# Optimization experiments

Measured on AMD Instinct MI355X. Metric: run time of the kernel, lower is better.

## Reference

```python
import jax, jax.numpy as jnp
import numpy as np
import math

E = 1024
H = 16
D = E // H  # head_dim = 64
B, T = 2, 2048


def setup_inputs() -> dict:
    key = jax.random.key(0)
    ks = jax.random.split(key, 10)
    s_in = 1.0 / math.sqrt(E)
    s_hd = 1.0 / math.sqrt(D)
    return {
        "hidden_states": jax.random.normal(ks[0], (B, T, E), dtype=jnp.float32),
        # stacked per-head Linear weights (torch Linear: y = x @ W.T + b)
        "Wq": jax.random.uniform(ks[1], (H, E, D), jnp.float32, -s_in, s_in),
        "bq": jax.random.uniform(ks[2], (H, D), jnp.float32, -s_in, s_in),
        "Wk": jax.random.uniform(ks[3], (H, E, D), jnp.float32, -s_in, s_in),
        "bk": jax.random.uniform(ks[4], (H, D), jnp.float32, -s_in, s_in),
        "Wv": jax.random.uniform(ks[5], (H, E, D), jnp.float32, -s_in, s_in),
        "bv": jax.random.uniform(ks[6], (H, D), jnp.float32, -s_in, s_in),
        "Wo": jax.random.uniform(ks[7], (H, D, E), jnp.float32, -s_hd, s_hd),
        "bo": jax.random.uniform(ks[8], (H, E), jnp.float32, -s_hd, s_hd),
        "gate": jnp.ones((H,), dtype=jnp.float32),
    }


def reference(hidden_states, Wq, bq, Wk, bk, Wv, bv, Wo, bo, gate):
    # Batched per-head projections: [B,T,E] x [H,E,D] -> [B,H,T,D]
    Q = jnp.einsum("bte,hed->bhtd", hidden_states, Wq) + bq[None, :, None, :]
    K = jnp.einsum("bte,hed->bhtd", hidden_states, Wk) + bk[None, :, None, :]
    V = jnp.einsum("bte,hed->bhtd", hidden_states, Wv) + bv[None, :, None, :]
    scale = 1.0 / math.sqrt(D)
    scores = jnp.einsum("bhtd,bhsd->bhts", Q, K) * scale  # [B,H,T,T]
    weights = jax.nn.softmax(scores, axis=-1)
    attn = jnp.einsum("bhts,bhsd->bhtd", weights, V)  # [B,H,T,D]
    # Per-head output proj (bias included before gating), gated, summed over heads
    proj = jnp.einsum("bhtd,hde->bhte", attn, Wo) + bo[None, :, None, :]
    out = jnp.sum(proj * gate[None, :, None, None], axis=1)  # [B,T,E]
    return out
```

## Files before the change

### kernel.cpp

```cpp
#include <hip/hip_runtime.h>
#include <math.h>

#define E_DIM 1024
#define H_DIM 16
#define D_DIM 64
#define B_DIM 2
#define T_DIM 2048
#define M_TOT (B_DIM * T_DIM)

typedef __bf16 bf16_t;
typedef bf16_t bf16x4 __attribute__((ext_vector_type(4)));
typedef bf16_t bf16x8 __attribute__((ext_vector_type(8)));
typedef float f32x4 __attribute__((ext_vector_type(4)));

#define LOG2E_DIV8 0.18033688011112042f

__device__ __forceinline__ float fast_exp2(float x) {
#if __has_builtin(__builtin_amdgcn_exp2f)
    return __builtin_amdgcn_exp2f(x);
#else
    return __expf(x * 0.6931471805599453f);
#endif
}

__device__ __forceinline__ void load_lds16(const void* g, void* l) {
    __builtin_amdgcn_global_load_lds(
        (const __attribute__((address_space(1))) unsigned int*)g,
        (__attribute__((address_space(3))) unsigned int*)l, 16, 0, 0);
}

__global__ __launch_bounds__(256) void prep_kernel(
    const float* __restrict__ x,
    const float* __restrict__ Wq, const float* __restrict__ Wk,
    const float* __restrict__ Wv, const float* __restrict__ Wo,
    const float* __restrict__ bo, const float* __restrict__ gate,
    bf16_t* __restrict__ Xb, bf16_t* __restrict__ Wcat,
    bf16_t* __restrict__ Wgt, float* __restrict__ bsum) {
    __shared__ float Tt[64][65];
    const int b = blockIdx.x;
    const int tid = threadIdx.x;

    if (b < 2048) {
        size_t i = ((size_t)b * 256 + tid) * 8;
        float4 a0 = *reinterpret_cast<const float4*>(x + i);
        float4 a1 = *reinterpret_cast<const float4*>(x + i + 4);
        bf16x8 o;
        o[0] = (bf16_t)a0.x; o[1] = (bf16_t)a0.y; o[2] = (bf16_t)a0.z; o[3] = (bf16_t)a0.w;
        o[4] = (bf16_t)a1.x; o[5] = (bf16_t)a1.y; o[6] = (bf16_t)a1.z; o[7] = (bf16_t)a1.w;
        *reinterpret_cast<bf16x8*>(Xb + i) = o;
    } else if (b < 2816) {
        const int idx = b - 2048;
        const int z = idx >> 8;
        const int rem = idx & 255;
        const int h = rem >> 4, et = rem & 15;
        const float* W = z == 0 ? Wq : (z == 1 ? Wk : Wv);
        const int r = tid >> 2, c4 = (tid & 3) * 16;
        const float* src = W + (size_t)h * 65536 + (size_t)(et * 64 + r) * 64 + c4;
        #pragma unroll
        for (int k = 0; k < 16; k += 4) {
            float4 v = *reinterpret_cast<const float4*>(src + k);
            Tt[r][c4 + k + 0] = v.x; Tt[r][c4 + k + 1] = v.y;
            Tt[r][c4 + k + 2] = v.z; Tt[r][c4 + k + 3] = v.w;
        }
        __syncthreads();
        bf16x8 o0, o1;
        #pragma unroll
        for (int k = 0; k < 8; ++k) o0[k] = (bf16_t)Tt[c4 + k][r];
        #pragma unroll
        for (int k = 0; k < 8; ++k) o1[k] = (bf16_t)Tt[c4 + 8 + k][r];
        bf16_t* dst = Wcat + ((size_t)(z * 16 + h) * 64 + r) * 1024 + et * 64 + c4;
        *reinterpret_cast<bf16x8*>(dst) = o0;
        *reinterpret_cast<bf16x8*>(dst + 8) = o1;
    } else if (b < 3072) {
        const int idx = b - 2816;
        const int h = idx >> 4, et = idx & 15;
        const float g = gate[h];
        const int r = tid >> 2, c4 = (tid & 3) * 16;
        const float* src = Wo + (size_t)h * 65536 + (size_t)r * 1024 + et * 64 + c4;
        #pragma unroll
        for (int k = 0; k < 16; k += 4) {
            float4 v = *reinterpret_cast<const float4*>(src + k);
            Tt[r][c4 + k + 0] = v.x * g; Tt[r][c4 + k + 1] = v.y * g;
            Tt[r][c4 + k + 2] = v.z * g; Tt[r][c4 + k + 3] = v.w * g;
        }
        __syncthreads();
        bf16x8 o0, o1;
        #pragma unroll
        for (int k = 0; k < 8; ++k) o0[k] = (bf16_t)Tt[c4 + k][r];
        #pragma unroll
        for (int k = 0; k < 8; ++k) o1[k] = (bf16_t)Tt[c4 + 8 + k][r];
        bf16_t* dst = Wgt + (size_t)(et * 64 + r) * 1024 + h * 64 + c4;
        *reinterpret_cast<bf16x8*>(dst) = o0;
        *reinterpret_cast<bf16x8*>(dst + 8) = o1;
    } else {
        const int e = (b - 3072) * 256 + tid;
        float s = 0.f;
        #pragma unroll
        for (int h = 0; h < H_DIM; ++h) s += gate[h] * bo[h * E_DIM + e];
        bsum[e] = s;
    }
}

__global__ __launch_bounds__(256) void qkv_gemm_kernel(
    const bf16_t* __restrict__ Xb, const bf16_t* __restrict__ Wcat,
    const float* __restrict__ bqp, const float* __restrict__ bkp,
    const float* __restrict__ bvp,
    bf16_t* __restrict__ Qw, bf16_t* __restrict__ Kw, bf16_t* __restrict__ Vtw) {
    const int p = blockIdx.x;
    const int l = (p & 7) * 96 + (p >> 3);
    const int mx = l & 31, ny = l >> 5;
    const int m0 = mx * 128, n0 = ny * 128;
    const int z = n0 >> 10;

    __shared__ bf16_t As[128][32];
    __shared__ bf16_t Bs[128][32];

    const int tid = threadIdx.x;
    const int lane = tid & 63, wid = tid >> 6;
    const int wr = wid >> 1, wc = wid & 1;
    const int lr = lane & 15, lg = lane >> 4;
    const int srow = lane >> 2, scol = (lane & 3) * 8;

    const int b_idx = m0 >> 11;
    const int t00 = m0 & (T_DIM - 1);

    #define QKV_STAGE(k0)                                                          \
        _Pragma("unroll")                                                          \
        for (int j = 0; j < 2; ++j) {                                              \
            load_lds16(Xb + (size_t)(m0 + wid * 32 + j * 16 + srow) * E_DIM + (k0) + scol, \
                       (char*)&As[0][0] + wid * 2048 + j * 1024);                  \
            load_lds16(Wcat + (size_t)(n0 + wid * 32 + j * 16 + srow) * E_DIM + (k0) + scol, \
                       (char*)&Bs[0][0] + wid * 2048 + j * 1024);                  \
        }
    #define QKV_FRAGS                                                              \
        bf16x8 a[4], bb[4];                                                        \
        _Pragma("unroll")                                                          \
        for (int i = 0; i < 4; ++i)                                                \
            a[i] = *reinterpret_cast<const bf16x8*>(&As[wr * 64 + i * 16 + lr][lg * 8]); \
        _Pragma("unroll")                                                          \
        for (int j = 0; j < 4; ++j)                                                \
            bb[j] = *reinterpret_cast<const bf16x8*>(&Bs[wc * 64 + j * 16 + lr][lg * 8]);

    if (z < 2) {
        f32x4 acc[4][4] = {};
        for (int k0 = 0; k0 < E_DIM; k0 += 32) {
            QKV_STAGE(k0);
            __syncthreads();
            QKV_FRAGS;
            __builtin_amdgcn_s_setprio(1);
            #pragma unroll
            for (int j = 0; j < 4; ++j)
                #pragma unroll
                for (int i = 0; i < 4; ++i)
                    acc[j][i] = __builtin_amdgcn_mfma_f32_16x16x32_bf16(bb[j], a[i], acc[j][i], 0, 0, 0);
            __builtin_amdgcn_s_setprio(0);
            __syncthreads();
        }
        const float scale = (z == 0) ? LOG2E_DIV8 : 1.0f;
        const float* bias = (z == 0) ? bqp : bkp;
        bf16_t* Obase = (z == 0) ? Qw : Kw;
        #pragma unroll
        for (int j = 0; j < 4; ++j) {
            const int n = n0 + wc * 64 + j * 16 + lg * 4;
            const int h = (n >> 6) & 15;
            const int dbase = n & 63;
            const float4 bv4 = *reinterpret_cast<const float4*>(&bias[n & 1023]);
            bf16_t* O = Obase + (size_t)(b_idx * H_DIM + h) * T_DIM * 64;
            #pragma unroll
            for (int i = 0; i < 4; ++i) {
                const int t = t00 + wr * 64 + i * 16 + lr;
                bf16x4 t4;
                #pragma unroll
                for (int r = 0; r < 4; ++r)
                    t4[r] = (bf16_t)((acc[j][i][r] + (&bv4.x)[r]) * scale);
                *reinterpret_cast<bf16x4*>(&O[(size_t)t * 64 + dbase]) = t4;
            }
        }
    } else {
        f32x4 acc[4][4] = {};
        for (int k0 = 0; k0 < E_DIM; k0 += 32) {
            QKV_STAGE(k0);
            __syncthreads();
            QKV_FRAGS;
            __builtin_amdgcn_s_setprio(1);
            #pragma unroll
            for (int i = 0; i < 4; ++i)
                #pragma unroll
                for (int j = 0; j < 4; ++j)
                    acc[i][j] = __builtin_amdgcn_mfma_f32_16x16x32_bf16(a[i], bb[j], acc[i][j], 0, 0, 0);
            __builtin_amdgcn_s_setprio(0);
            __syncthreads();
        }
        #pragma unroll
        for (int j = 0; j < 4; ++j) {
            const int n = n0 + wc * 64 + j * 16 + lr;
            const int h = (n >> 6) & 15;
            const int d = n & 63;
            const float bval = bvp[n & 1023];
            bf16_t* O = Vtw + (size_t)(b_idx * H_DIM + h) * 64 * T_DIM + (size_t)d * T_DIM;
            #pragma unroll
            for (int i = 0; i < 4; ++i) {
                const int t = t00 + wr * 64 + i * 16 + lg * 4;
                bf16x4 t4;
                #pragma unroll
                for (int r = 0; r < 4; ++r) t4[r] = (bf16_t)(acc[i][j][r] + bval);
                *reinterpret_cast<bf16x4*>(&O[t]) = t4;
            }
        }
    }
    #undef QKV_STAGE
    #undef QKV_FRAGS
}

__global__ __launch_bounds__(512, 4) void attn_mfma_kernel(
    const bf16_t* __restrict__ Q, const bf16_t* __restrict__ K,
    const bf16_t* __restrict__ Vt, bf16_t* __restrict__ Aw) {
    const int p = blockIdx.x;
    const int l = (p & 7) * 64 + (p >> 3);
    const int qx = l & 15, bh = l >> 4;
    const int b_idx = bh >> 4, h = bh & 15;
    const int q0 = qx * 128;
    const size_t base = (size_t)bh * T_DIM * 64;

    __shared__ bf16_t Ks[128][72];
    __shared__ bf16_t Vs[64][136];
    __shared__ bf16_t Ps[8][16][136];

    const int tid = threadIdx.x;
    const int lane = tid & 63;
    const int wid = tid >> 6;
    const int lr = lane & 15, lg = lane >> 4;

    bf16x8 bq[2];
    #pragma unroll
    for (int kc = 0; kc < 2; ++kc)
        bq[kc] = *reinterpret_cast<const bf16x8*>(
            Q + base + (size_t)(q0 + wid * 16 + lr) * 64 + kc * 32 + lg * 8);

    const int kr = tid >> 2, kc0 = (tid & 3) * 16;
    const int vr = tid >> 3, vc0 = (tid & 7) * 16;

    float mreg = -INFINITY, lrow = 0.f;
    f32x4 o[4] = {};

    for (int s0 = 0; s0 < T_DIM; s0 += 128) {
        {
            const bf16_t* ksrc = K + base + (size_t)(s0 + kr) * 64 + kc0;
            bf16x8 k0 = *reinterpret_cast<const bf16x8*>(ksrc);
            bf16x8 k1 = *reinterpret_cast<const bf16x8*>(ksrc + 8);
            const bf16_t* vsrc = Vt + base + (size_t)vr * T_DIM + s0 + vc0;
            bf16x8 v0 = *reinterpret_cast<const bf16x8*>(vsrc);
            bf16x8 v1 = *reinterpret_cast<const bf16x8*>(vsrc + 8);
            *reinterpret_cast<bf16x8*>(&Ks[kr][kc0])     = k0;
            *reinterpret_cast<bf16x8*>(&Ks[kr][kc0 + 8]) = k1;
            *reinterpret_cast<bf16x8*>(&Vs[vr][vc0])     = v0;
            *reinterpret_cast<bf16x8*>(&Vs[vr][vc0 + 8]) = v1;
        }
        __syncthreads();

        f32x4 s[8] = {};
        __builtin_amdgcn_s_setprio(1);
        #pragma unroll
        for (int kb = 0; kb < 8; ++kb)
            #pragma unroll
            for (int kc = 0; kc < 2; ++kc) {
                bf16x8 ak = *reinterpret_cast<const bf16x8*>(&Ks[kb * 16 + lr][kc * 32 + lg * 8]);
                s[kb] = __builtin_amdgcn_mfma_f32_16x16x32_bf16(ak, bq[kc], s[kb], 0, 0, 0);
            }
        __builtin_amdgcn_s_setprio(0);

        float pmax = -INFINITY;
        #pragma unroll
        for (int kb = 0; kb < 8; ++kb)
            pmax = fmaxf(pmax,
                   fmaxf(fmaxf(s[kb][0], s[kb][1]), fmaxf(s[kb][2], s[kb][3])));
        pmax = fmaxf(pmax, __shfl_xor(pmax, 16));
        pmax = fmaxf(pmax, __shfl_xor(pmax, 32));

        if (__any(pmax > mreg + 11.5f)) {
            float newm = fmaxf(mreg, pmax);
            float alpha = fast_exp2(mreg - newm);
            mreg = newm;
            lrow *= alpha;
            #pragma unroll
            for (int db = 0; db < 4; ++db) o[db] *= alpha;
        }

        float rs = 0.f;
        #pragma unroll
        for (int kb = 0; kb < 8; ++kb) {
            bf16x4 t4;
            #pragma unroll
            for (int r = 0; r < 4; ++r) {
                float pv = fast_exp2(s[kb][r] - mreg);
                rs += pv;
                t4[r] = (bf16_t)pv;
            }
            *reinterpret_cast<bf16x4*>(&Ps[wid][lr][kb * 16 + lg * 4]) = t4;
        }
        rs += __shfl_xor(rs, 16);
        rs += __shfl_xor(rs, 32);
        lrow += rs;

        __builtin_amdgcn_s_setprio(1);
        #pragma unroll
        for (int sc = 0; sc < 4; ++sc) {
            bf16x8 bp = *reinterpret_cast<const bf16x8*>(&Ps[wid][lr][sc * 32 + lg * 8]);
            #pragma unroll
            for (int db = 0; db < 4; ++db) {
                bf16x8 av = *reinterpret_cast<const bf16x8*>(&Vs[db * 16 + lr][sc * 32 + lg * 8]);
                o[db] = __builtin_amdgcn_mfma_f32_16x16x32_bf16(av, bp, o[db], 0, 0, 0);
            }
        }
        __builtin_amdgcn_s_setprio(0);
        __syncthreads();
    }

    const float linv = 1.f / lrow;
    const int t = q0 + wid * 16 + lr;
    const size_t rowbase = ((size_t)b_idx * T_DIM + t) * E_DIM + h * 64;
    #pragma unroll
    for (int db = 0; db < 4; ++db) {
        bf16x4 t4;
        #pragma unroll
        for (int r = 0; r < 4; ++r) t4[r] = (bf16_t)(o[db][r] * linv);
        *reinterpret_cast<bf16x4*>(&Aw[rowbase + db * 16 + lg * 4]) = t4;
    }
}

__global__ __launch_bounds__(256) void out_gemm_kernel(
    const bf16_t* __restrict__ Aw, const bf16_t* __restrict__ Wgt,
    const float* __restrict__ bsum, float* __restrict__ out) {
    const int p = blockIdx.x;
    const int l = (p & 7) * 64 + (p >> 3);
    const int mx = l & 31, ny = l >> 5;
    const int m0 = mx * 128, n0 = ny * 64;

    __shared__ bf16_t As[128][32];
    __shared__ bf16_t Bs[64][32];

    const int tid = threadIdx.x;
    const int lane = tid & 63, wid = tid >> 6;
    const int wr = wid >> 1, wc = wid & 1;
    const int lr = lane & 15, lg = lane >> 4;
    const int srow = lane >> 2, scol = (lane & 3) * 8;

    f32x4 acc[2][4] = {};

    for (int k0 = 0; k0 < E_DIM; k0 += 32) {
        #pragma unroll
        for (int j = 0; j < 2; ++j)
            load_lds16(Aw + (size_t)(m0 + wid * 32 + j * 16 + srow) * E_DIM + k0 + scol,
                       (char*)&As[0][0] + wid * 2048 + j * 1024);
        load_lds16(Wgt + (size_t)(n0 + wid * 16 + srow) * E_DIM + k0 + scol,
                   (char*)&Bs[0][0] + wid * 1024);
        __syncthreads();
        bf16x8 a[4], bb[2];
        #pragma unroll
        for (int i = 0; i < 4; ++i)
            a[i] = *reinterpret_cast<const bf16x8*>(&As[wr * 64 + i * 16 + lr][lg * 8]);
        #pragma unroll
        for (int j = 0; j < 2; ++j)
            bb[j] = *reinterpret_cast<const bf16x8*>(&Bs[wc * 32 + j * 16 + lr][lg * 8]);
        __builtin_amdgcn_s_setprio(1);
        #pragma unroll
        for (int j = 0; j < 2; ++j)
            #pragma unroll
            for (int i = 0; i < 4; ++i)
                acc[j][i] = __builtin_amdgcn_mfma_f32_16x16x32_bf16(bb[j], a[i], acc[j][i], 0, 0, 0);
        __builtin_amdgcn_s_setprio(0);
        __syncthreads();
    }

    #pragma unroll
    for (int j = 0; j < 2; ++j) {
        const int e = n0 + wc * 32 + j * 16 + lg * 4;
        const float4 bs4 = *reinterpret_cast<const float4*>(&bsum[e]);
        #pragma unroll
        for (int i = 0; i < 4; ++i) {
            const int m = m0 + wr * 64 + i * 16 + lr;
            float4 o4;
            o4.x = acc[j][i][0] + bs4.x;
            o4.y = acc[j][i][1] + bs4.y;
            o4.z = acc[j][i][2] + bs4.z;
            o4.w = acc[j][i][3] + bs4.w;
            *reinterpret_cast<float4*>(&out[(size_t)m * E_DIM + e]) = o4;
        }
    }
}

extern "C" void kernel_launch(void* const* d_in, const int* in_sizes, int n_in,
                              void* d_out, int out_size, void* d_ws, size_t ws_size,
                              hipStream_t stream) {
    const float* hs   = (const float*)d_in[0];
    const float* Wq   = (const float*)d_in[1];
    const float* bq   = (const float*)d_in[2];
    const float* Wk   = (const float*)d_in[3];
    const float* bk   = (const float*)d_in[4];
    const float* Wv   = (const float*)d_in[5];
    const float* bv   = (const float*)d_in[6];
    const float* Wo   = (const float*)d_in[7];
    const float* bo   = (const float*)d_in[8];
    const float* gate = (const float*)d_in[9];
    float* out = (float*)d_out;

    const size_t NX = (size_t)M_TOT * E_DIM;
    const size_t NW = (size_t)H_DIM * D_DIM * E_DIM;
    bf16_t* p = (bf16_t*)d_ws;
    bf16_t* Xb   = p; p += NX;
    bf16_t* Wcat = p; p += 3 * NW;
    bf16_t* Wgt  = p; p += NW;
    bf16_t* Qw   = p; p += NX;
    bf16_t* Kw   = p; p += NX;
    bf16_t* Vtw  = p; p += NX;
    bf16_t* Aw   = p; p += NX;
    float*  bsum = (float*)p;

    prep_kernel<<<dim3(3076), 256, 0, stream>>>(hs, Wq, Wk, Wv, Wo, bo, gate,
                                                Xb, Wcat, Wgt, bsum);

    qkv_gemm_kernel<<<dim3(768), 256, 0, stream>>>(Xb, Wcat, bq, bk, bv, Qw, Kw, Vtw);

    attn_mfma_kernel<<<dim3(512), 512, 0, stream>>>(Qw, Kw, Vtw, Aw);

    out_gemm_kernel<<<dim3(512), 256, 0, stream>>>(Aw, Wgt, bsum, out);
}
```

Measured before the change: 205.5 us.

## Switch attention to 32x32 MFMA with register-resident P via lane swaps

Rewrites the attention kernel to use 32x32x16 bf16 MFMA tiles with 4 waves each owning 32 query rows, and a 64-key tile per iteration. The softmax probabilities are repacked in registers with cross-half shuffles so they feed straight into the PV MFMA, which removes the LDS round-trip through the Ps buffer. The aim is fewer LDS accesses and higher MFMA efficiency. In exchange there are smaller key tiles, so twice as many block barriers, fewer threads per block, and more register pressure from the 16-wide accumulators.

```diff
diff --git a/kernel.cpp b/kernel.cpp
--- a/kernel.cpp
+++ b/kernel.cpp
@@ -9,9 +9,12 @@
 #define M_TOT (B_DIM * T_DIM)
 
 typedef __bf16 bf16_t;
+typedef bf16_t bf16x2 __attribute__((ext_vector_type(2)));
 typedef bf16_t bf16x4 __attribute__((ext_vector_type(4)));
 typedef bf16_t bf16x8 __attribute__((ext_vector_type(8)));
 typedef float f32x4 __attribute__((ext_vector_type(4)));
+typedef float f32x16 __attribute__((ext_vector_type(16)));
+typedef unsigned int uint4v __attribute__((ext_vector_type(4)));
 
 #define LOG2E_DIV8 0.18033688011112042f
 
@@ -21,6 +24,19 @@
 #else
     return __expf(x * 0.6931471805599453f);
 #endif
+}
+
+__device__ __forceinline__ unsigned pack_bf16x2(float a, float b) {
+    bf16x2 t = {(bf16_t)a, (bf16_t)b};
+    return __builtin_bit_cast(unsigned, t);
+}
+
+__device__ __forceinline__ void swap32(unsigned& a, unsigned& b, int hi) {
+    unsigned as = (unsigned)__shfl_xor((int)a, 32);
+    unsigned bs = (unsigned)__shfl_xor((int)b, 32);
+    unsigned na = hi ? bs : a;
+    unsigned nb = hi ? b : as;
+    a = na; b = nb;
 }
 
 __device__ __forceinline__ void load_lds16(const void* g, void* l) {
@@ -212,7 +228,7 @@
     #undef QKV_FRAGS
 }
 
-__global__ __launch_bounds__(512, 4) void attn_mfma_kernel(
+__global__ __launch_bounds__(256, 3) void attn_mfma_kernel(
     const bf16_t* __restrict__ Q, const bf16_t* __restrict__ K,
     const bf16_t* __restrict__ Vt, bf16_t* __restrict__ Aw) {
     const int p = blockIdx.x;
@@ -222,59 +238,61 @@
     const int q0 = qx * 128;
     const size_t base = (size_t)bh * T_DIM * 64;
 
-    __shared__ bf16_t Ks[128][72];
-    __shared__ bf16_t Vs[64][136];
-    __shared__ bf16_t Ps[8][16][136];
+    __shared__ bf16_t Ks[64][72];
+    __shared__ bf16_t Vs[64][72];
 
     const int tid = threadIdx.x;
     const int lane = tid & 63;
-    const int wid = tid >> 6;
-    const int lr = lane & 15, lg = lane >> 4;
-
-    bf16x8 bq[2];
+    const int w = tid >> 6;
+    const int lq = lane & 31;
+    const int hi = lane >> 5;
+
+    const int qrow = q0 + w * 32 + lq;
+    bf16x8 qb[4];
     #pragma unroll
-    for (int kc = 0; kc < 2; ++kc)
-        bq[kc] = *reinterpret_cast<const bf16x8*>(
-            Q + base + (size_t)(q0 + wid * 16 + lr) * 64 + kc * 32 + lg * 8);
-
-    const int kr = tid >> 2, kc0 = (tid & 3) * 16;
-    const int vr = tid >> 3, vc0 = (tid & 7) * 16;
+    for (int kc = 0; kc < 4; ++kc)
+        qb[kc] = *reinterpret_cast<const bf16x8*>(
+            Q + base + (size_t)qrow * 64 + kc * 16 + hi * 8);
+
+    const int sr = tid >> 2, sc = (tid & 3) * 16;
 
     float mreg = -INFINITY, lrow = 0.f;
-    f32x4 o[4] = {};
-
-    for (int s0 = 0; s0 < T_DIM; s0 += 128) {
+    f32x16 o[2] = {};
+
+    for (int s0 = 0; s0 < T_DIM; s0 += 64) {
         {
-            const bf16_t* ksrc = K + base + (size_t)(s0 + kr) * 64 + kc0;
+            const bf16_t* ksrc = K + base + (size_t)(s0 + sr) * 64 + sc;
             bf16x8 k0 = *reinterpret_cast<const bf16x8*>(ksrc);
             bf16x8 k1 = *reinterpret_cast<const bf16x8*>(ksrc + 8);
-            const bf16_t* vsrc = Vt + base + (size_t)vr * T_DIM + s0 + vc0;
+            const bf16_t* vsrc = Vt + base + (size_t)sr * T_DIM + s0 + sc;
             bf16x8 v0 = *reinterpret_cast<const bf16x8*>(vsrc);
             bf16x8 v1 = *reinterpret_cast<const bf16x8*>(vsrc + 8);
-            *reinterpret_cast<bf16x8*>(&Ks[kr][kc0])     = k0;
-            *reinterpret_cast<bf16x8*>(&Ks[kr][kc0 + 8]) = k1;
-            *reinterpret_cast<bf16x8*>(&Vs[vr][vc0])     = v0;
-            *reinterpret_cast<bf16x8*>(&Vs[vr][vc0 + 8]) = v1;
-        }
-        __syncthreads();
-
-        f32x4 s[8] = {};
+            *reinterpret_cast<bf16x8*>(&Ks[sr][sc])     = k0;
+            *reinterpret_cast<bf16x8*>(&Ks[sr][sc + 8]) = k1;
+            *reinterpret_cast<bf16x8*>(&Vs[sr][sc])     = v0;
+            *reinterpret_cast<bf16x8*>(&Vs[sr][sc + 8]) = v1;
+        }
+        __syncthreads();
+
+        f32x16 s32[2] = {};
         __builtin_amdgcn_s_setprio(1);
         #pragma unroll
-        for (int kb = 0; kb < 8; ++kb)
-            #pragma unroll
-            for (int kc = 0; kc < 2; ++kc) {
-                bf16x8 ak = *reinterpret_cast<const bf16x8*>(&Ks[kb * 16 + lr][kc * 32 + lg * 8]);
-                s[kb] = __builtin_amdgcn_mfma_f32_16x16x32_bf16(ak, bq[kc], s[kb], 0, 0, 0);
+        for (int sb = 0; sb < 2; ++sb)
+            #pragma unroll
+            for (int kc = 0; kc < 4; ++kc) {
+                bf16x8 ka = *reinterpret_cast<const bf16x8*>(
+                    &Ks[sb * 32 + lq][kc * 16 + hi * 8]);
+                s32[sb] = __builtin_amdgcn_mfma_f32_32x32x16_bf16(ka, qb[kc], s32[sb], 0, 0, 0);
             }
         __builtin_amdgcn_s_setprio(0);
 
         float pmax = -INFINITY;
         #pragma unroll
-        for (int kb = 0; kb < 8; ++kb)
-            pmax = fmaxf(pmax,
-                   fmaxf(fmaxf(s[kb][0], s[kb][1]), fmaxf(s[kb][2], s[kb][3])));
-        pmax = fmaxf(pmax, __shfl_xor(pmax, 16));
+        for (int sb = 0; sb < 2; ++sb)
+            #pragma unroll
+            for (int r = 0; r < 16; r += 4)
+                pmax = fmaxf(pmax, fmaxf(fmaxf(s32[sb][r], s32[sb][r + 1]),
+                                         fmaxf(s32[sb][r + 2], s32[sb][r + 3])));
         pmax = fmaxf(pmax, __shfl_xor(pmax, 32));
 
         if (__any(pmax > mreg + 11.5f)) {
@@ -282,50 +300,66 @@
             float alpha = fast_exp2(mreg - newm);
             mreg = newm;
             lrow *= alpha;
-            #pragma unroll
-            for (int db = 0; db < 4; ++db) o[db] *= alpha;
+            o[0] *= alpha;
+            o[1] *= alpha;
         }
 
         float rs = 0.f;
-        #pragma unroll
-        for (int kb = 0; kb < 8; ++kb) {
-            bf16x4 t4;
-            #pragma unroll
-            for (int r = 0; r < 4; ++r) {
-                float pv = fast_exp2(s[kb][r] - mreg);
-                rs += pv;
-                t4[r] = (bf16_t)pv;
-            }
-            *reinterpret_cast<bf16x4*>(&Ps[wid][lr][kb * 16 + lg * 4]) = t4;
-        }
-        rs += __shfl_xor(rs, 16);
+        unsigned W[2][4][2];
+        #pragma unroll
+        for (int sb = 0; sb < 2; ++sb)
+            #pragma unroll
+            for (int grp = 0; grp < 4; ++grp) {
+                float p0 = fast_exp2(s32[sb][grp * 4 + 0] - mreg);
+                float p1 = fast_exp2(s32[sb][grp * 4 + 1] - mreg);
+                float p2 = fast_exp2(s32[sb][grp * 4 + 2] - mreg);
+                float p3 = fast_exp2(s32[sb][grp * 4 + 3] - mreg);
+                rs += (p0 + p1) + (p2 + p3);
+                W[sb][grp][0] = pack_bf16x2(p0, p1);
+                W[sb][grp][1] = pack_bf16x2(p2, p3);
+            }
         rs += __shfl_xor(rs, 32);
         lrow += rs;
 
+        bf16x8 pa[4];
+        #pragma unroll
+        for (int sb = 0; sb < 2; ++sb)
+            #pragma unroll
+            for (int kl = 0; kl < 2; ++kl) {
+                unsigned a0 = W[sb][2 * kl][0], b0 = W[sb][2 * kl + 1][0];
+                unsigned a1 = W[sb][2 * kl][1], b1 = W[sb][2 * kl + 1][1];
+                swap32(a0, b0, hi);
+                swap32(a1, b1, hi);
+                uint4v tv = {a0, a1, b0, b1};
+                pa[sb * 2 + kl] = __builtin_bit_cast(bf16x8, tv);
+            }
+
         __builtin_amdgcn_s_setprio(1);
         #pragma unroll
-        for (int sc = 0; sc < 4; ++sc) {
-            bf16x8 bp = *reinterpret_cast<const bf16x8*>(&Ps[wid][lr][sc * 32 + lg * 8]);
-            #pragma unroll
-            for (int db = 0; db < 4; ++db) {
-                bf16x8 av = *reinterpret_cast<const bf16x8*>(&Vs[db * 16 + lr][sc * 32 + lg * 8]);
-                o[db] = __builtin_amdgcn_mfma_f32_16x16x32_bf16(av, bp, o[db], 0, 0, 0);
-            }
-        }
+        for (int ks = 0; ks < 4; ++ks)
+            #pragma unroll
+            for (int db = 0; db < 2; ++db) {
+                bf16x8 va = *reinterpret_cast<const bf16x8*>(
+                    &Vs[db * 32 + lq][ks * 16 + hi * 8]);
+                o[db] = __builtin_amdgcn_mfma_f32_32x32x16_bf16(va, pa[ks], o[db], 0, 0, 0);
+            }
         __builtin_amdgcn_s_setprio(0);
         __syncthreads();
     }
 
     const float linv = 1.f / lrow;
-    const int t = q0 + wid * 16 + lr;
-    const size_t rowbase = ((size_t)b_idx * T_DIM + t) * E_DIM + h * 64;
+    const size_t rowbase = ((size_t)b_idx * T_DIM + qrow) * E_DIM + h * 64;
     #pragma unroll
-    for (int db = 0; db < 4; ++db) {
-        bf16x4 t4;
-        #pragma unroll
-        for (int r = 0; r < 4; ++r) t4[r] = (bf16_t)(o[db][r] * linv);
-        *reinterpret_cast<bf16x4*>(&Aw[rowbase + db * 16 + lg * 4]) = t4;
-    }
+    for (int db = 0; db < 2; ++db)
+        #pragma unroll
+        for (int grp = 0; grp < 4; ++grp) {
+            bf16x4 t4;
+            #pragma unroll
+            for (int i = 0; i < 4; ++i)
+                t4[i] = (bf16_t)(o[db][grp * 4 + i] * linv);
+            *reinterpret_cast<bf16x4*>(
+                &Aw[rowbase + db * 32 + grp * 8 + hi * 4]) = t4;
+        }
 }
 
 __global__ __launch_bounds__(256) void out_gemm_kernel(
@@ -421,7 +455,7 @@
 
     qkv_gemm_kernel<<<dim3(768), 256, 0, stream>>>(Xb, Wcat, bq, bk, bv, Qw, Kw, Vtw);
 
-    attn_mfma_kernel<<<dim3(512), 512, 0, stream>>>(Qw, Kw, Vtw, Aw);
+    attn_mfma_kernel<<<dim3(512), 256, 0, stream>>>(Qw, Kw, Vtw, Aw);
 
     out_gemm_kernel<<<dim3(512), 256, 0, stream>>>(Aw, Wgt, bsum, out);
 }
```

Result: no change. 203.8 us (-0.8%).
